# Performance work log

Measured on AMD Instinct MI355X. Metric: run time of the kernel, lower is better.

## Reference

```python
import jax, jax.numpy as jnp
import numpy as np
from jax import lax

DIM = 512
DH = 16          # dim_head
H = DIM // DH    # 32 heads
WS = 7           # window_size
SR = 3           # sr_ratio (AvgPool2d kernel, stride=1)
EPS = 1e-5


def _rel_pos_indices():
    # mirrors the torch buffer construction, incl. the [:, 24:] slice for sr_ratio>1
    pos = np.arange(WS)
    gi, gj = np.meshgrid(pos, pos, indexing='ij')
    grid = np.stack([gi, gj], axis=-1).reshape(-1, 2)            # (49, 2)
    rel = grid[:, None, :] - grid[None, :, :] + (WS - 1)         # (49, 49, 2)
    idx = rel[..., 0] * (2 * WS - 1) + rel[..., 1]               # (49, 49)
    return jnp.asarray(idx[:, 24:], dtype=jnp.int32)             # (49, 25)


def _layernorm(x, g, b):
    m = jnp.mean(x, axis=-1, keepdims=True)
    v = jnp.mean(jnp.square(x - m), axis=-1, keepdims=True)
    return (x - m) * lax.rsqrt(v + EPS) * g + b


def setup_inputs() -> dict:
    key = jax.random.key(0)
    ks = jax.random.split(key, 8)
    B, X, Y = 8, 14, 14
    x = jax.random.normal(ks[0], (B, X, Y, WS, WS, DIM), dtype=jnp.float32)
    ln_gamma = 1.0 + 0.1 * jax.random.normal(ks[1], (DIM,), dtype=jnp.float32)
    ln_beta = 0.1 * jax.random.normal(ks[2], (DIM,), dtype=jnp.float32)
    s = 1.0 / np.sqrt(DIM)
    Wq = jax.random.normal(ks[3], (DIM, DIM), dtype=jnp.float32) * s
    Wkv = jax.random.normal(ks[4], (2 * DIM, DIM), dtype=jnp.float32) * s
    Wout = jax.random.normal(ks[5], (DIM, DIM), dtype=jnp.float32) * s
    rel_pos_emb = 0.02 * jax.random.normal(ks[6], ((2 * WS - 1) ** 2, H), dtype=jnp.float32)
    return {"x": x, "ln_gamma": ln_gamma, "ln_beta": ln_beta,
            "Wq": Wq, "Wkv": Wkv, "Wout": Wout, "rel_pos_emb": rel_pos_emb}


def reference(x, ln_gamma, ln_beta, Wq, Wkv, Wout, rel_pos_emb):
    B, X, Y, W1, W2, D = x.shape
    Nw = B * X * Y                      # number of windows
    Nq = W1 * W2                        # 49 query tokens per window
    xn = _layernorm(x, ln_gamma, ln_beta)
    xw = xn.reshape(Nw, Nq, D)
    # queries
    q = (xw @ Wq.T).reshape(Nw, Nq, H, DH).transpose(0, 2, 1, 3) * (DH ** -0.5)  # (Nw,H,Nq,DH)
    # KV spatial reduction: AvgPool2d(kernel=SR, stride=1) over the 7x7 window
    xi = xw.reshape(Nw, W1, W2, D)
    xp = lax.reduce_window(xi, 0.0, lax.add, (1, SR, SR, 1), (1, 1, 1, 1), 'VALID') / (SR * SR)
    Hp, Wp = W1 - SR + 1, W2 - SR + 1   # 5, 5
    xkv = _layernorm(xp.reshape(Nw, Hp * Wp, D), ln_gamma, ln_beta)
    # to_kv with einops '(dim h l)' decomposition: last axis factored as (DH, H, 2)
    kv = (xkv @ Wkv.T).reshape(Nw, Hp * Wp, DH, H, 2)
    k = kv[..., 0].transpose(0, 3, 1, 2)  # (Nw, H, Nk, DH)
    v = kv[..., 1].transpose(0, 3, 1, 2)
    sim = jnp.einsum('bhid,bhjd->bhij', q, k)                    # (Nw,H,49,25)
    bias = rel_pos_emb[_rel_pos_indices()]                       # (49,25,H)
    sim = sim + bias.transpose(2, 0, 1)[None]
    attn = jax.nn.softmax(sim, axis=-1)
    out = jnp.einsum('bhij,bhjd->bhid', attn, v)                 # (Nw,H,49,DH)
    out = out.reshape(Nw, H, W1, W2, DH).transpose(0, 2, 3, 1, 4).reshape(Nw, W1, W2, D)
    out = out @ Wout.T
    return out.reshape(B, X, Y, W1, W2, D)
```

## Files before the change

### kernel.cpp

```cpp
#include <hip/hip_runtime.h>

typedef _Float16 half8 __attribute__((ext_vector_type(8)));
typedef float f32x4 __attribute__((ext_vector_type(4)));

#define MFMA16(a,b,c) __builtin_amdgcn_mfma_f32_16x16x32_f16(a,b,c,0,0,0)
#define GLOAD16(g, l) __builtin_amdgcn_global_load_lds( \
  (const __attribute__((address_space(1))) void*)(g), \
  (__attribute__((address_space(3))) void*)(l), 16, 0, 0)

static constexpr int NW     = 1568;
static constexpr int MROWSQ = 76832;
static constexpr int MPADQ  = 76928;
static constexpr int MROWKV = 39200;
static constexpr int MPADKV = 39296;

__device__ __forceinline__ half8 h8z(){
  half8 z = {(_Float16)0,(_Float16)0,(_Float16)0,(_Float16)0,
             (_Float16)0,(_Float16)0,(_Float16)0,(_Float16)0};
  return z;
}

__global__ void k_prep_w(const float* __restrict__ a, const float* __restrict__ b,
                         const float* __restrict__ c,
                         _Float16* __restrict__ ah, _Float16* __restrict__ bh,
                         _Float16* __restrict__ ch){
  int i = blockIdx.x*256 + threadIdx.x;
  if(i < 262144) ah[i] = (_Float16)(a[i]*0.25f);
  int j = i - 262144;
  if(j >= 0 && j < 524288) bh[j] = (_Float16)b[j];
  int k = i - 786432;
  if(k >= 0 && k < 262144) ch[k] = (_Float16)c[k];
}

__global__ void k_prep_bias(const float* __restrict__ rel, float* __restrict__ biasT){
  int t = blockIdx.x*256 + threadIdx.x;
  if(t >= 65536) return;
  int h = t >> 11;
  int r = t & 2047;
  int i = r >> 5, slotk = r & 31;
  int kg = slotk >> 3, idx = slotk & 7;
  int j = (idx < 4) ? (kg*4 + idx) : (16 + kg*4 + idx - 4);
  float v = 0.f;
  if(j >= 25) v = -1e30f;
  else if(i < 49){
    int qi = i/7, qj = i%7;
    int c = j + 24, ki = c/7, kj = c%7;
    v = rel[((qi-ki+6)*13 + (qj-kj+6))*32 + h];
  }
  biasT[t] = v;
}

__global__ __launch_bounds__(512) void k_ln_pool(const float* __restrict__ x,
    const float* __restrict__ gamma, const float* __restrict__ beta,
    _Float16* __restrict__ xn, _Float16* __restrict__ xkv){
  __shared__ _Float16 nrm[49*512];
  const int w = blockIdx.x, t = threadIdx.x;
  const int lane = t & 63, wv = t >> 6;
  float gf[8], bf[8];
  {
    float4 g0 = *(const float4*)(gamma + lane*8);
    float4 g1 = *(const float4*)(gamma + lane*8 + 4);
    float4 b0 = *(const float4*)(beta  + lane*8);
    float4 b1 = *(const float4*)(beta  + lane*8 + 4);
    gf[0]=g0.x; gf[1]=g0.y; gf[2]=g0.z; gf[3]=g0.w;
    gf[4]=g1.x; gf[5]=g1.y; gf[6]=g1.z; gf[7]=g1.w;
    bf[0]=b0.x; bf[1]=b0.y; bf[2]=b0.z; bf[3]=b0.w;
    bf[4]=b1.x; bf[5]=b1.y; bf[6]=b1.z; bf[7]=b1.w;
  }
  const float* xw = x + (size_t)w*49*512;
  for(int i = wv; i < 49; i += 8){
    const float* row = xw + i*512 + lane*8;
    float4 v0 = *(const float4*)row;
    float4 v1 = *(const float4*)(row+4);
    float v[8] = {v0.x,v0.y,v0.z,v0.w,v1.x,v1.y,v1.z,v1.w};
    float s = 0.f, sq = 0.f;
    #pragma unroll
    for(int j=0;j<8;j++){ s += v[j]; sq += v[j]*v[j]; }
    #pragma unroll
    for(int o=32;o>=1;o>>=1){ s += __shfl_xor(s,o); sq += __shfl_xor(sq,o); }
    float mean = s*(1.f/512.f);
    float rstd = rsqrtf(sq*(1.f/512.f) - mean*mean + 1e-5f);
    half8 nh;
    #pragma unroll
    for(int j=0;j<8;j++)
      nh[j] = (_Float16)((v[j]-mean)*rstd*gf[j] + bf[j]);
    *(half8*)&nrm[i*512 + lane*8] = nh;
    *(half8*)(xn + ((size_t)w*49 + i)*512 + lane*8) = nh;
  }
  __syncthreads();
  for(int p = wv; p < 25; p += 8){
    const int pi = p/5, pj = p%5;
    float acc[8] = {0,0,0,0,0,0,0,0};
    #pragma unroll
    for(int a=0;a<3;a++)
      #pragma unroll
      for(int bb=0;bb<3;bb++){
        half8 rv = *(const half8*)&nrm[((pi+a)*7 + (pj+bb))*512 + lane*8];
        #pragma unroll
        for(int j=0;j<8;j++) acc[j] += (float)rv[j];
      }
    float s = 0.f, sq = 0.f;
    #pragma unroll
    for(int j=0;j<8;j++){ acc[j] *= (1.f/9.f); s += acc[j]; sq += acc[j]*acc[j]; }
    #pragma unroll
    for(int o=32;o>=1;o>>=1){ s += __shfl_xor(s,o); sq += __shfl_xor(sq,o); }
    float mean = s*(1.f/512.f);
    float rstd = rsqrtf(sq*(1.f/512.f) - mean*mean + 1e-5f);
    half8 nh;
    #pragma unroll
    for(int j=0;j<8;j++) nh[j] = (_Float16)((acc[j]-mean)*rstd*gf[j] + bf[j]);
    *(half8*)(xkv + ((size_t)w*25 + p)*512 + lane*8) = nh;
  }
}

template<int MODE>
__global__ __launch_bounds__(256) void k_gemm(const _Float16* __restrict__ A,
    const _Float16* __restrict__ Bw, _Float16* __restrict__ oh,
    float* __restrict__ of, int ldc, int ntn, int nwg){
  __shared__ __align__(16) _Float16 As[2][128*32];
  __shared__ __align__(16) _Float16 Bs[2][128*32];
  const int orig = blockIdx.x;
  const int xcd = orig & 7, slot = orig >> 3;
  const int q8 = nwg >> 3, r8 = nwg & 7;
  const int base = (xcd < r8) ? xcd*(q8+1) : r8*(q8+1) + (xcd-r8)*q8;
  const int lin = base + slot;
  const int m0 = (lin / ntn) * 128, n0 = (lin % ntn) * 128;
  const int t = threadIdx.x, lane = t & 63;
  const int wid = t >> 6, wm = (wid>>1)*64, wn = (wid&1)*64;
  const int lr = lane & 15, kg = lane >> 4;
  const _Float16* Ab = A  + (size_t)m0*512;
  const _Float16* Bb = Bw + (size_t)n0*512;
  const int foff0 = wid*64, foff1 = 256 + wid*64;
  const int f0 = foff0 + lane, f1 = foff1 + lane;
  const size_t ga0 = (size_t)(f0>>2)*512 + (f0&3)*8;
  const size_t ga1 = (size_t)(f1>>2)*512 + (f1&3)*8;

  GLOAD16(Ab + ga0, &As[0][foff0*8]);
  GLOAD16(Bb + ga0, &Bs[0][foff0*8]);
  GLOAD16(Ab + ga1, &As[0][foff1*8]);
  GLOAD16(Bb + ga1, &Bs[0][foff1*8]);
  __syncthreads();

  f32x4 acc[4][4] = {};
  int cur = 0;
  for(int kt = 0; kt < 16; ++kt){
    if(kt < 15){
      const int k0 = (kt+1)*32;
      GLOAD16(Ab + ga0 + k0, &As[cur^1][foff0*8]);
      GLOAD16(Bb + ga0 + k0, &Bs[cur^1][foff0*8]);
      GLOAD16(Ab + ga1 + k0, &As[cur^1][foff1*8]);
      GLOAD16(Bb + ga1 + k0, &Bs[cur^1][foff1*8]);
    }
    half8 af[4], bf[4];
    #pragma unroll
    for(int mt=0;mt<4;mt++) af[mt] = *(const half8*)&As[cur][(wm + mt*16 + lr)*32 + kg*8];
    #pragma unroll
    for(int nt=0;nt<4;nt++) bf[nt] = *(const half8*)&Bs[cur][(wn + nt*16 + lr)*32 + kg*8];
    #pragma unroll
    for(int mt=0;mt<4;mt++)
      #pragma unroll
      for(int nt=0;nt<4;nt++)
        acc[mt][nt] = MFMA16(af[mt], bf[nt], acc[mt][nt]);
    __syncthreads();
    cur ^= 1;
  }
  #pragma unroll
  for(int mt=0;mt<4;mt++)
    #pragma unroll
    for(int nt=0;nt<4;nt++)
      #pragma unroll
      for(int r=0;r<4;r++){
        int row = m0 + wm + mt*16 + kg*4 + r;
        int col = n0 + wn + nt*16 + lr;
        float vv = acc[mt][nt][r];
        if(MODE == 0){
          oh[(size_t)row*ldc + col] = (_Float16)vv;
        } else {
          if(row < MROWSQ) of[(size_t)row*ldc + col] = vv;
        }
      }
}

__global__ __launch_bounds__(256) void k_repack(const _Float16* __restrict__ kvb,
    _Float16* __restrict__ kb, _Float16* __restrict__ vb){
  __shared__ uint2 s2[6400];
  uint32_t* su = (uint32_t*)s2;
  const int w = blockIdx.x, t = threadIdx.x;
  const uint2* src = (const uint2*)(kvb + (size_t)w*25*1024);
  #pragma unroll
  for(int it=0; it<25; ++it){
    int U = it*256 + t;
    int j = U >> 8, u = U & 255;
    s2[j*256 + (u ^ (u>>4) ^ (j&15))] = src[U];
  }
  __syncthreads();
  _Float16* kdst = kb + (size_t)w*12800;
  _Float16* vdst = vb + (size_t)w*12800;
  for(int it=0; it<7; ++it){
    int q = it*256 + t;
    if(q < 1600){
      int h = q/50, rem = q%50, j = rem>>1, half = rem&1;
      half8 k8, v8;
      #pragma unroll
      for(int jj=0;jj<8;jj++){
        int dh = half*8 + jj;
        int slot = j*256 + ((dh*16 + (h>>1)) ^ dh ^ (j&15));
        uint32_t val = su[slot*2 + (h&1)];
        k8[jj] = ((_Float16*)&val)[0];
        v8[jj] = ((_Float16*)&val)[1];
      }
      *(half8*)(kdst + q*8) = k8;
      *(half8*)(vdst + q*8) = v8;
    }
  }
}

__global__ __launch_bounds__(256) void k_attn(const _Float16* __restrict__ q,
    const _Float16* __restrict__ kb, const _Float16* __restrict__ vb,
    const float* __restrict__ biasT, _Float16* __restrict__ ao){
  const int w = blockIdx.x, hi = blockIdx.y, t = threadIdx.x;
  const int lane = t & 63, wv = t >> 6;
  const int lr = lane & 15, kg = lane >> 4;
  const size_t qbase = ((size_t)w*49)*512;
  const int hA = hi*4 + wv;
  const size_t kvA = (((size_t)w*32 + hA)*25)*16;
  const size_t kvB = kvA + 6400;
  half8 kA0=h8z(), kA1=h8z(), kB0=h8z(), kB1=h8z();
  if(kg < 2){
    kA0 = *(const half8*)(kb + kvA + lr*16 + kg*8);
    kB0 = *(const half8*)(kb + kvB + lr*16 + kg*8);
    if(lr < 9){
      kA1 = *(const half8*)(kb + kvA + (16+lr)*16 + kg*8);
      kB1 = *(const half8*)(kb + kvB + (16+lr)*16 + kg*8);
    }
  }
  half8 qA[4], qB[4];
  #pragma unroll
  for(int qt=0;qt<4;qt++){
    if(kg < 2){
      const _Float16* p = q + qbase + (size_t)(qt*16+lr)*512 + hA*16 + kg*8;
      qA[qt] = *(const half8*)p;
      qB[qt] = *(const half8*)(p + 256);
    } else { qA[qt] = h8z(); qB[qt] = h8z(); }
  }
  half8 vA = h8z(), vB = h8z();
  #pragma unroll
  for(int idx=0; idx<8; idx++){
    int key = (idx<4) ? (kg*4+idx) : (16 + kg*4 + idx-4);
    if(key < 25){
      vA[idx] = vb[kvA + key*16 + lr];
      vB[idx] = vb[kvB + key*16 + lr];
    }
  }
  const float4* btA = (const float4*)(biasT + (size_t)hA*2048);
  const float4* btB = (const float4*)(biasT + (size_t)(hA+16)*2048);
  #pragma unroll
  for(int qt=0;qt<4;qt++){
    f32x4 sA0={}, sA1={}, sB0={}, sB1={};
    sA0 = MFMA16(kA0, qA[qt], sA0);
    sA1 = MFMA16(kA1, qA[qt], sA1);
    sB0 = MFMA16(kB0, qB[qt], sB0);
    sB1 = MFMA16(kB1, qB[qt], sB1);
    const int i = qt*16 + lr;
    const int bidx = i*8 + kg*2;
    float4 bA0 = btA[bidx], bA1 = btA[bidx+1];
    float4 bB0 = btB[bidx], bB1 = btB[bidx+1];
    float a[8], b[8];
    a[0]=sA0[0]+bA0.x; a[1]=sA0[1]+bA0.y; a[2]=sA0[2]+bA0.z; a[3]=sA0[3]+bA0.w;
    a[4]=sA1[0]+bA1.x; a[5]=sA1[1]+bA1.y; a[6]=sA1[2]+bA1.z; a[7]=sA1[3]+bA1.w;
    b[0]=sB0[0]+bB0.x; b[1]=sB0[1]+bB0.y; b[2]=sB0[2]+bB0.z; b[3]=sB0[3]+bB0.w;
    b[4]=sB1[0]+bB1.x; b[5]=sB1[1]+bB1.y; b[6]=sB1[2]+bB1.z; b[7]=sB1[3]+bB1.w;
    float mA = a[0], mB = b[0];
    #pragma unroll
    for(int j=1;j<8;j++){ mA = fmaxf(mA, a[j]); mB = fmaxf(mB, b[j]); }
    mA = fmaxf(mA, __shfl_xor(mA,16)); mB = fmaxf(mB, __shfl_xor(mB,16));
    mA = fmaxf(mA, __shfl_xor(mA,32)); mB = fmaxf(mB, __shfl_xor(mB,32));
    float sumA = 0.f, sumB = 0.f;
    #pragma unroll
    for(int j=0;j<8;j++){
      a[j] = __expf(a[j]-mA); sumA += a[j];
      b[j] = __expf(b[j]-mB); sumB += b[j];
    }
    sumA += __shfl_xor(sumA,16); sumB += __shfl_xor(sumB,16);
    sumA += __shfl_xor(sumA,32); sumB += __shfl_xor(sumB,32);
    float invA = 1.f/sumA, invB = 1.f/sumB;
    half8 pA, pB;
    #pragma unroll
    for(int j=0;j<8;j++){
      pA[j] = (_Float16)(a[j]*invA);
      pB[j] = (_Float16)(b[j]*invB);
    }
    f32x4 oA={}, oB={};
    oA = MFMA16(pA, vA, oA);
    oB = MFMA16(pB, vB, oB);
    #pragma unroll
    for(int r=0;r<4;r++){
      int qi2 = qt*16 + kg*4 + r;
      if(qi2 < 49){
        _Float16* dst = ao + qbase + (size_t)qi2*512 + hA*16 + lr;
        dst[0]   = (_Float16)oA[r];
        dst[256] = (_Float16)oB[r];
      }
    }
  }
}

extern "C" void kernel_launch(void* const* d_in, const int* in_sizes, int n_in,
                              void* d_out, int out_size, void* d_ws, size_t ws_size,
                              hipStream_t stream){
  (void)in_sizes; (void)n_in; (void)out_size; (void)ws_size;
  const float* x    = (const float*)d_in[0];
  const float* gam  = (const float*)d_in[1];
  const float* bet  = (const float*)d_in[2];
  const float* Wq   = (const float*)d_in[3];
  const float* Wkv  = (const float*)d_in[4];
  const float* Wout = (const float*)d_in[5];
  const float* rel  = (const float*)d_in[6];
  float* out = (float*)d_out;

  char* ws = (char*)d_ws;
  size_t off = 0;
  auto alloc = [&](size_t n){ char* p = ws + off; off += (n + 1023) & ~(size_t)1023; return p; };
  _Float16* xn    = (_Float16*)alloc((size_t)MPADQ*512*2);
  _Float16* xkv   = (_Float16*)alloc((size_t)MPADKV*512*2);
  _Float16* kvb   = (_Float16*)alloc((size_t)MPADKV*1024*2);
  _Float16* kbuf  = (_Float16*)alloc((size_t)NW*32*25*16*2);
  _Float16* vbuf  = (_Float16*)alloc((size_t)NW*32*25*16*2);
  _Float16* wqh   = (_Float16*)alloc((size_t)262144*2);
  _Float16* wkvh  = (_Float16*)alloc((size_t)524288*2);
  _Float16* wouth = (_Float16*)alloc((size_t)262144*2);
  float*    biasT = (float*)   alloc((size_t)65536*4);
  _Float16* qb    = kvb;

  k_prep_w   <<<dim3(4096), 256, 0, stream>>>(Wq, Wkv, Wout, wqh, wkvh, wouth);
  k_prep_bias<<<dim3(256),  256, 0, stream>>>(rel, biasT);
  k_ln_pool  <<<dim3(NW),   512, 0, stream>>>(x, gam, bet, xn, xkv);
  k_gemm<0>  <<<dim3(2456), 256, 0, stream>>>(xkv, wkvh,  kvb, nullptr, 1024, 8, 2456);
  k_repack   <<<dim3(NW),   256, 0, stream>>>(kvb, kbuf, vbuf);
  k_gemm<0>  <<<dim3(2404), 256, 0, stream>>>(xn,  wqh,   qb,  nullptr,  512, 4, 2404);
  k_attn     <<<dim3(NW,4), 256, 0, stream>>>(qb, kbuf, vbuf, biasT, xn);
  k_gemm<1>  <<<dim3(2404), 256, 0, stream>>>(xn,  wouth, nullptr, out,  512, 4, 2404);
}
```

Before: 396.2 us.

## Fuse attention with output projection via LDS-staged per-window tile

Attention and the output projection now run in one kernel with one block per window. The block writes the 49x512 attention result into a swizzled LDS tile, then each of 8 waves multiplies it by a 64-column slice of Wout and writes fp32 output directly. This removes the fp16 round trip of the attention output through global memory and one kernel launch. In exchange, Wout is read from global or L2 by every window without LDS staging, the GEMM has no double buffering, and 64KB of LDS per block limits occupancy.

```diff
diff --git a/kernel.cpp b/kernel.cpp
--- a/kernel.cpp
+++ b/kernel.cpp
@@ -113,10 +113,9 @@
   }
 }
 
-template<int MODE>
 __global__ __launch_bounds__(256) void k_gemm(const _Float16* __restrict__ A,
     const _Float16* __restrict__ Bw, _Float16* __restrict__ oh,
-    float* __restrict__ of, int ldc, int ntn, int nwg){
+    int ldc, int ntn, int nwg){
   __shared__ __align__(16) _Float16 As[2][128*32];
   __shared__ __align__(16) _Float16 Bs[2][128*32];
   const int orig = blockIdx.x;
@@ -172,12 +171,7 @@
       for(int r=0;r<4;r++){
         int row = m0 + wm + mt*16 + kg*4 + r;
         int col = n0 + wn + nt*16 + lr;
-        float vv = acc[mt][nt][r];
-        if(MODE == 0){
-          oh[(size_t)row*ldc + col] = (_Float16)vv;
-        } else {
-          if(row < MROWSQ) of[(size_t)row*ldc + col] = vv;
-        }
+        oh[(size_t)row*ldc + col] = (_Float16)acc[mt][nt][r];
       }
 }
 
@@ -215,94 +209,133 @@
   }
 }
 
-__global__ __launch_bounds__(256) void k_attn(const _Float16* __restrict__ q,
+__global__ __launch_bounds__(512) void k_attn_out(const _Float16* __restrict__ q,
     const _Float16* __restrict__ kb, const _Float16* __restrict__ vb,
-    const float* __restrict__ biasT, _Float16* __restrict__ ao){
-  const int w = blockIdx.x, hi = blockIdx.y, t = threadIdx.x;
+    const float* __restrict__ biasT, const _Float16* __restrict__ wo,
+    float* __restrict__ out){
+  __shared__ _Float16 Olds[64*512];
+  const int w = blockIdx.x, t = threadIdx.x;
   const int lane = t & 63, wv = t >> 6;
   const int lr = lane & 15, kg = lane >> 4;
   const size_t qbase = ((size_t)w*49)*512;
-  const int hA = hi*4 + wv;
-  const size_t kvA = (((size_t)w*32 + hA)*25)*16;
-  const size_t kvB = kvA + 6400;
-  half8 kA0=h8z(), kA1=h8z(), kB0=h8z(), kB1=h8z();
-  if(kg < 2){
-    kA0 = *(const half8*)(kb + kvA + lr*16 + kg*8);
-    kB0 = *(const half8*)(kb + kvB + lr*16 + kg*8);
-    if(lr < 9){
-      kA1 = *(const half8*)(kb + kvA + (16+lr)*16 + kg*8);
-      kB1 = *(const half8*)(kb + kvB + (16+lr)*16 + kg*8);
-    }
-  }
-  half8 qA[4], qB[4];
+  for(int z = t; z < 960; z += 512){
+    int row = 49 + z/64, c8 = z%64;
+    *(half8*)&Olds[row*512 + c8*8] = h8z();
+  }
+  #pragma unroll 2
+  for(int it=0; it<2; ++it){
+    const int hA = wv + it*8;
+    const size_t kvA = (((size_t)w*32 + hA)*25)*16;
+    const size_t kvB = kvA + 6400;
+    half8 kA0=h8z(), kA1=h8z(), kB0=h8z(), kB1=h8z();
+    if(kg < 2){
+      kA0 = *(const half8*)(kb + kvA + lr*16 + kg*8);
+      kB0 = *(const half8*)(kb + kvB + lr*16 + kg*8);
+      if(lr < 9){
+        kA1 = *(const half8*)(kb + kvA + (16+lr)*16 + kg*8);
+        kB1 = *(const half8*)(kb + kvB + (16+lr)*16 + kg*8);
+      }
+    }
+    half8 qA[4], qB[4];
+    #pragma unroll
+    for(int qt=0;qt<4;qt++){
+      if(kg < 2){
+        const _Float16* p = q + qbase + (size_t)(qt*16+lr)*512 + hA*16 + kg*8;
+        qA[qt] = *(const half8*)p;
+        qB[qt] = *(const half8*)(p + 256);
+      } else { qA[qt] = h8z(); qB[qt] = h8z(); }
+    }
+    half8 vA = h8z(), vB = h8z();
+    #pragma unroll
+    for(int idx=0; idx<8; idx++){
+      int key = (idx<4) ? (kg*4+idx) : (16 + kg*4 + idx-4);
+      if(key < 25){
+        vA[idx] = vb[kvA + key*16 + lr];
+        vB[idx] = vb[kvB + key*16 + lr];
+      }
+    }
+    const float4* btA = (const float4*)(biasT + (size_t)hA*2048);
+    const float4* btB = (const float4*)(biasT + (size_t)(hA+16)*2048);
+    #pragma unroll
+    for(int qt=0;qt<4;qt++){
+      f32x4 sA0={}, sA1={}, sB0={}, sB1={};
+      sA0 = MFMA16(kA0, qA[qt], sA0);
+      sA1 = MFMA16(kA1, qA[qt], sA1);
+      sB0 = MFMA16(kB0, qB[qt], sB0);
+      sB1 = MFMA16(kB1, qB[qt], sB1);
+      const int i = qt*16 + lr;
+      const int bidx = i*8 + kg*2;
+      float4 bA0 = btA[bidx], bA1 = btA[bidx+1];
+      float4 bB0 = btB[bidx], bB1 = btB[bidx+1];
+      float a[8], b[8];
+      a[0]=sA0[0]+bA0.x; a[1]=sA0[1]+bA0.y; a[2]=sA0[2]+bA0.z; a[3]=sA0[3]+bA0.w;
+      a[4]=sA1[0]+bA1.x; a[5]=sA1[1]+bA1.y; a[6]=sA1[2]+bA1.z; a[7]=sA1[3]+bA1.w;
+      b[0]=sB0[0]+bB0.x; b[1]=sB0[1]+bB0.y; b[2]=sB0[2]+bB0.z; b[3]=sB0[3]+bB0.w;
+      b[4]=sB1[0]+bB1.x; b[5]=sB1[1]+bB1.y; b[6]=sB1[2]+bB1.z; b[7]=sB1[3]+bB1.w;
+      float mA = a[0], mB = b[0];
+      #pragma unroll
+      for(int j=1;j<8;j++){ mA = fmaxf(mA, a[j]); mB = fmaxf(mB, b[j]); }
+      mA = fmaxf(mA, __shfl_xor(mA,16)); mB = fmaxf(mB, __shfl_xor(mB,16));
+      mA = fmaxf(mA, __shfl_xor(mA,32)); mB = fmaxf(mB, __shfl_xor(mB,32));
+      float sumA = 0.f, sumB = 0.f;
+      #pragma unroll
+      for(int j=0;j<8;j++){
+        a[j] = __expf(a[j]-mA); sumA += a[j];
+        b[j] = __expf(b[j]-mB); sumB += b[j];
+      }
+      sumA += __shfl_xor(sumA,16); sumB += __shfl_xor(sumB,16);
+      sumA += __shfl_xor(sumA,32); sumB += __shfl_xor(sumB,32);
+      float invA = 1.f/sumA, invB = 1.f/sumB;
+      half8 pA, pB;
+      #pragma unroll
+      for(int j=0;j<8;j++){
+        pA[j] = (_Float16)(a[j]*invA);
+        pB[j] = (_Float16)(b[j]*invB);
+      }
+      f32x4 oA={}, oB={};
+      oA = MFMA16(pA, vA, oA);
+      oB = MFMA16(pB, vB, oB);
+      #pragma unroll
+      for(int r=0;r<4;r++){
+        int qi2 = qt*16 + kg*4 + r;
+        if(qi2 < 49){
+          int sw = (qi2&7)<<3;
+          Olds[qi2*512 + ((hA*16 + lr)       ^ sw)] = (_Float16)oA[r];
+          Olds[qi2*512 + ((hA*16 + 256 + lr) ^ sw)] = (_Float16)oB[r];
+        }
+      }
+    }
+  }
+  __syncthreads();
+  f32x4 acc[4][4] = {};
+  const _Float16* wb = wo + (size_t)(wv*64)*512;
+  for(int ks=0; ks<16; ++ks){
+    half8 af[4], bf[4];
+    #pragma unroll
+    for(int mt=0;mt<4;mt++){
+      int row = mt*16 + lr;
+      int ch = (ks*32 + kg*8) ^ ((row&7)<<3);
+      af[mt] = *(const half8*)&Olds[row*512 + ch];
+    }
+    #pragma unroll
+    for(int nt=0;nt<4;nt++)
+      bf[nt] = *(const half8*)(wb + (size_t)(nt*16+lr)*512 + ks*32 + kg*8);
+    #pragma unroll
+    for(int mt=0;mt<4;mt++)
+      #pragma unroll
+      for(int nt=0;nt<4;nt++)
+        acc[mt][nt] = MFMA16(af[mt], bf[nt], acc[mt][nt]);
+  }
   #pragma unroll
-  for(int qt=0;qt<4;qt++){
-    if(kg < 2){
-      const _Float16* p = q + qbase + (size_t)(qt*16+lr)*512 + hA*16 + kg*8;
-      qA[qt] = *(const half8*)p;
-      qB[qt] = *(const half8*)(p + 256);
-    } else { qA[qt] = h8z(); qB[qt] = h8z(); }
-  }
-  half8 vA = h8z(), vB = h8z();
-  #pragma unroll
-  for(int idx=0; idx<8; idx++){
-    int key = (idx<4) ? (kg*4+idx) : (16 + kg*4 + idx-4);
-    if(key < 25){
-      vA[idx] = vb[kvA + key*16 + lr];
-      vB[idx] = vb[kvB + key*16 + lr];
-    }
-  }
-  const float4* btA = (const float4*)(biasT + (size_t)hA*2048);
-  const float4* btB = (const float4*)(biasT + (size_t)(hA+16)*2048);
-  #pragma unroll
-  for(int qt=0;qt<4;qt++){
-    f32x4 sA0={}, sA1={}, sB0={}, sB1={};
-    sA0 = MFMA16(kA0, qA[qt], sA0);
-    sA1 = MFMA16(kA1, qA[qt], sA1);
-    sB0 = MFMA16(kB0, qB[qt], sB0);
-    sB1 = MFMA16(kB1, qB[qt], sB1);
-    const int i = qt*16 + lr;
-    const int bidx = i*8 + kg*2;
-    float4 bA0 = btA[bidx], bA1 = btA[bidx+1];
-    float4 bB0 = btB[bidx], bB1 = btB[bidx+1];
-    float a[8], b[8];
-    a[0]=sA0[0]+bA0.x; a[1]=sA0[1]+bA0.y; a[2]=sA0[2]+bA0.z; a[3]=sA0[3]+bA0.w;
-    a[4]=sA1[0]+bA1.x; a[5]=sA1[1]+bA1.y; a[6]=sA1[2]+bA1.z; a[7]=sA1[3]+bA1.w;
-    b[0]=sB0[0]+bB0.x; b[1]=sB0[1]+bB0.y; b[2]=sB0[2]+bB0.z; b[3]=sB0[3]+bB0.w;
-    b[4]=sB1[0]+bB1.x; b[5]=sB1[1]+bB1.y; b[6]=sB1[2]+bB1.z; b[7]=sB1[3]+bB1.w;
-    float mA = a[0], mB = b[0];
-    #pragma unroll
-    for(int j=1;j<8;j++){ mA = fmaxf(mA, a[j]); mB = fmaxf(mB, b[j]); }
-    mA = fmaxf(mA, __shfl_xor(mA,16)); mB = fmaxf(mB, __shfl_xor(mB,16));
-    mA = fmaxf(mA, __shfl_xor(mA,32)); mB = fmaxf(mB, __shfl_xor(mB,32));
-    float sumA = 0.f, sumB = 0.f;
-    #pragma unroll
-    for(int j=0;j<8;j++){
-      a[j] = __expf(a[j]-mA); sumA += a[j];
-      b[j] = __expf(b[j]-mB); sumB += b[j];
-    }
-    sumA += __shfl_xor(sumA,16); sumB += __shfl_xor(sumB,16);
-    sumA += __shfl_xor(sumA,32); sumB += __shfl_xor(sumB,32);
-    float invA = 1.f/sumA, invB = 1.f/sumB;
-    half8 pA, pB;
-    #pragma unroll
-    for(int j=0;j<8;j++){
-      pA[j] = (_Float16)(a[j]*invA);
-      pB[j] = (_Float16)(b[j]*invB);
-    }
-    f32x4 oA={}, oB={};
-    oA = MFMA16(pA, vA, oA);
-    oB = MFMA16(pB, vB, oB);
-    #pragma unroll
-    for(int r=0;r<4;r++){
-      int qi2 = qt*16 + kg*4 + r;
-      if(qi2 < 49){
-        _Float16* dst = ao + qbase + (size_t)qi2*512 + hA*16 + lr;
-        dst[0]   = (_Float16)oA[r];
-        dst[256] = (_Float16)oB[r];
-      }
-    }
-  }
+  for(int mt=0;mt<4;mt++)
+    #pragma unroll
+    for(int nt=0;nt<4;nt++)
+      #pragma unroll
+      for(int r=0;r<4;r++){
+        int row = mt*16 + kg*4 + r;
+        if(row < 49)
+          out[((size_t)w*49 + row)*512 + wv*64 + nt*16 + lr] = acc[mt][nt][r];
+      }
 }
 
 extern "C" void kernel_launch(void* const* d_in, const int* in_sizes, int n_in,
@@ -335,9 +368,8 @@
   k_prep_w   <<<dim3(4096), 256, 0, stream>>>(Wq, Wkv, Wout, wqh, wkvh, wouth);
   k_prep_bias<<<dim3(256),  256, 0, stream>>>(rel, biasT);
   k_ln_pool  <<<dim3(NW),   512, 0, stream>>>(x, gam, bet, xn, xkv);
-  k_gemm<0>  <<<dim3(2456), 256, 0, stream>>>(xkv, wkvh,  kvb, nullptr, 1024, 8, 2456);
+  k_gemm     <<<dim3(2456), 256, 0, stream>>>(xkv, wkvh, kvb, 1024, 8, 2456);
   k_repack   <<<dim3(NW),   256, 0, stream>>>(kvb, kbuf, vbuf);
-  k_gemm<0>  <<<dim3(2404), 256, 0, stream>>>(xn,  wqh,   qb,  nullptr,  512, 4, 2404);
-  k_attn     <<<dim3(NW,4), 256, 0, stream>>>(qb, kbuf, vbuf, biasT, xn);
-  k_gemm<1>  <<<dim3(2404), 256, 0, stream>>>(xn,  wouth, nullptr, out,  512, 4, 2404);
-}
+  k_gemm     <<<dim3(2404), 256, 0, stream>>>(xn,  wqh,  qb,   512, 4, 2404);
+  k_attn_out <<<dim3(NW),   512, 0, stream>>>(qb, kbuf, vbuf, biasT, wouth, out);
+}
```

Measured after the change: 451.4 us. +13.9%, slower.
